# Kernel optimization log

Measured on AMD Instinct MI355X. Metric: run time of the kernel, lower is better.

## Reference

```python
import jax, jax.numpy as jnp
import numpy as np


def ternarize(w):
    """TWN ternarization: delta=0.7*mean|w|, alpha = mean of |w| over kept entries."""
    aw = jnp.abs(w)
    delta = 0.7 * jnp.mean(aw)
    mask = (aw > delta).astype(w.dtype)
    alpha = jnp.sum(aw * mask) / jnp.maximum(jnp.sum(mask), 1.0)
    return alpha * jnp.sign(w) * mask


def conv3x3(x, w):
    # NCHW input, OIHW weight, stride 1, padding 1
    return jax.lax.conv_general_dilated(
        x, w, window_strides=(1, 1), padding=((1, 1), (1, 1)),
        dimension_numbers=("NCHW", "OIHW", "NCHW"))


def maxpool2(x):
    return jax.lax.reduce_window(
        x, -jnp.inf, jax.lax.max,
        window_dimensions=(1, 1, 2, 2), window_strides=(1, 1, 2, 2),
        padding="VALID")


def setup_inputs() -> dict:
    key = jax.random.key(0)
    ks = jax.random.split(key, 9)
    B = 4096
    return {
        "x":   jax.random.normal(ks[0], (B, 3, 32, 32), dtype=jnp.float32),
        "w1":  jax.random.normal(ks[1], (16, 3, 3, 3), dtype=jnp.float32) * 0.1,
        "b1":  jax.random.normal(ks[2], (16,), dtype=jnp.float32) * 0.01,
        "w2":  jax.random.normal(ks[3], (32, 16, 3, 3), dtype=jnp.float32) * 0.1,
        "b2":  jax.random.normal(ks[4], (32,), dtype=jnp.float32) * 0.01,
        "wf1": jax.random.normal(ks[5], (128, 32 * 8 * 8), dtype=jnp.float32) * 0.05,
        "bf1": jax.random.normal(ks[6], (128,), dtype=jnp.float32) * 0.01,
        "wf2": jax.random.normal(ks[7], (10, 128), dtype=jnp.float32) * 0.05,
        "bf2": jax.random.normal(ks[8], (10,), dtype=jnp.float32) * 0.01,
    }


def reference(x, w1, b1, w2, b2, wf1, bf1, wf2, bf2):
    h = jax.nn.relu(conv3x3(x, ternarize(w1)) + b1[None, :, None, None])
    h = maxpool2(h)                                    # [B,16,16,16]
    h = jax.nn.relu(conv3x3(h, ternarize(w2)) + b2[None, :, None, None])
    h = maxpool2(h)                                    # [B,32,8,8]
    h = h.reshape(-1, 32 * 8 * 8)
    h = jax.nn.relu(h @ ternarize(wf1).T + bf1)        # [B,128]
    return h @ ternarize(wf2).T + bf2                  # [B,10]
```

## Files before the change

kernel.cpp:

```cpp
#include <hip/hip_runtime.h>
#include <math.h>


typedef _Float16 half2v __attribute__((ext_vector_type(2)));
typedef _Float16 half4  __attribute__((ext_vector_type(4)));
typedef _Float16 half8  __attribute__((ext_vector_type(8)));
typedef float    f32x4  __attribute__((ext_vector_type(4)));
typedef unsigned u32x2  __attribute__((ext_vector_type(2)));

#define WF1_N 262144
#define WF1_SLICES 64
#define WF1_SLICE 4096

__device__ __forceinline__ float block_reduce_256(float v, float* red, int t) {
    red[t] = v; __syncthreads();
    for (int o = 128; o > 0; o >>= 1) {
        if (t < o) red[t] += red[t + o];
        __syncthreads();
    }
    float r = red[0]; __syncthreads();
    return r;
}

__device__ __forceinline__ unsigned pk16(float a, float b) {
    half2v h;
    h[0] = (_Float16)a;
    h[1] = (_Float16)b;
    return __builtin_bit_cast(unsigned, h);
}

__global__ void tern_stageA(const float* __restrict__ w1,
                            const float* __restrict__ w2,
                            const float* __restrict__ wf1,
                            const float* __restrict__ wf2,
                            _Float16* __restrict__ tw1f,
                            _Float16* __restrict__ tw2f,
                            float* __restrict__ twf2,
                            float* __restrict__ part_sum) {
    __shared__ float red[256];
    const int t = threadIdx.x;
    const int bid = blockIdx.x;

    if (bid < WF1_SLICES) {
        const float4* src = reinterpret_cast<const float4*>(wf1 + (size_t)bid * WF1_SLICE);
        float s = 0.f;
#pragma unroll
        for (int j = 0; j < 4; ++j) {
            const float4 v = src[t + j * 256];
            s += fabsf(v.x) + fabsf(v.y) + fabsf(v.z) + fabsf(v.w);
        }
        const float tot = block_reduce_256(s, red, t);
        if (t == 0) part_sum[bid] = tot;
        return;
    }

    const float* w;
    int n;
    const int which = bid - WF1_SLICES;
    switch (which) {
        case 0: w = w1;  n = 432;  break;
        case 1: w = w2;  n = 4608; break;
        default: w = wf2; n = 1280; break;
    }
    float s = 0.f;
    for (int i = t; i < n; i += 256) s += fabsf(w[i]);
    const float delta = 0.7f * block_reduce_256(s, red, t) / (float)n;
    float sa = 0.f, cnt = 0.f;
    for (int i = t; i < n; i += 256) {
        float a = fabsf(w[i]);
        if (a > delta) { sa += a; cnt += 1.f; }
    }
    const float tot_sa = block_reduce_256(sa, red, t);
    const float tot_cnt = block_reduce_256(cnt, red, t);
    const float alpha = tot_sa / fmaxf(tot_cnt, 1.0f);

    switch (which) {
        case 0:
            for (int o = t; o < 768; o += 256) {
                int j = o & 3;
                int l = (o >> 2) & 63;
                int m = o >> 8;
                int rho = m * 4 + (l >> 4);
                int co = l & 15;
                float v = 0.f;
                if (rho < 9 && j < 3) {
                    float wv = w1[co * 27 + (rho / 3) * 9 + (rho % 3) * 3 + j];
                    v = (fabsf(wv) > delta) ? copysignf(alpha, wv) : 0.f;
                }
                tw1f[o] = (_Float16)v;
            }
            break;
        case 1:
            for (int o = t; o < 4608; o += 256) {
                int j  = o & 3;
                int ll = (o >> 2) & 63;
                int nt = (o >> 8) & 1;
                int s9 = o >> 9;
                int ci = (ll >> 4) * 4 + j;
                int co = (ll & 15) + nt * 16;
                float wv = w2[(co * 16 + ci) * 9 + s9];
                float v = (fabsf(wv) > delta) ? copysignf(alpha, wv) : 0.f;
                tw2f[o] = (_Float16)v;
            }
            break;
        default:
            for (int o = t; o < 1280; o += 256) {
                float wv = wf2[o];
                twf2[o] = (fabsf(wv) > delta) ? copysignf(alpha, wv) : 0.f;
            }
            break;
    }
}

__global__ void tern_stageB(const float* __restrict__ wf1,
                            const float* __restrict__ part_sum,
                            float* __restrict__ part_sa,
                            float* __restrict__ part_cnt) {
    __shared__ float red[256];
    const int t = threadIdx.x;
    const int bid = blockIdx.x;

    float v = (t < WF1_SLICES) ? part_sum[t] : 0.f;
    const float delta = 0.7f * block_reduce_256(v, red, t) / (float)WF1_N;

    const float4* src = reinterpret_cast<const float4*>(wf1 + (size_t)bid * WF1_SLICE);
    float sa = 0.f, cnt = 0.f;
#pragma unroll
    for (int j = 0; j < 4; ++j) {
        const float4 w4 = src[t + j * 256];
        float a;
        a = fabsf(w4.x); if (a > delta) { sa += a; cnt += 1.f; }
        a = fabsf(w4.y); if (a > delta) { sa += a; cnt += 1.f; }
        a = fabsf(w4.z); if (a > delta) { sa += a; cnt += 1.f; }
        a = fabsf(w4.w); if (a > delta) { sa += a; cnt += 1.f; }
    }
    const float tot_sa = block_reduce_256(sa, red, t);
    const float tot_cnt = block_reduce_256(cnt, red, t);
    if (t == 0) { part_sa[bid] = tot_sa; part_cnt[bid] = tot_cnt; }
}

__global__ void tern_stageC(const float* __restrict__ wf1,
                            const float* __restrict__ part_sum,
                            const float* __restrict__ part_sa,
                            const float* __restrict__ part_cnt,
                            _Float16* __restrict__ twf1) {
    __shared__ float red[256];
    const int t = threadIdx.x;

    float v = (t < WF1_SLICES) ? part_sum[t] : 0.f;
    const float delta = 0.7f * block_reduce_256(v, red, t) / (float)WF1_N;
    v = (t < WF1_SLICES) ? part_sa[t] : 0.f;
    const float tot_sa = block_reduce_256(v, red, t);
    v = (t < WF1_SLICES) ? part_cnt[t] : 0.f;
    const float tot_cnt = block_reduce_256(v, red, t);
    const float alpha = tot_sa / fmaxf(tot_cnt, 1.0f);

    const int tid = blockIdx.x * 256 + t;
    const float4 w4 = reinterpret_cast<const float4*>(wf1)[tid];
    half4 hv;
    hv[0] = (_Float16)((fabsf(w4.x) > delta) ? copysignf(alpha, w4.x) : 0.f);
    hv[1] = (_Float16)((fabsf(w4.y) > delta) ? copysignf(alpha, w4.y) : 0.f);
    hv[2] = (_Float16)((fabsf(w4.z) > delta) ? copysignf(alpha, w4.z) : 0.f);
    hv[3] = (_Float16)((fabsf(w4.w) > delta) ? copysignf(alpha, w4.w) : 0.f);
    reinterpret_cast<half4*>(twf1)[tid] = hv;
}

#define H1P 18
#define PSZ 3472
#define H1SZ (18*18*H1P)

__global__ __launch_bounds__(256, 5)
void conv12_kernel(const float* __restrict__ x,
                   const float* __restrict__ b1,
                   const float* __restrict__ b2,
                   const _Float16* __restrict__ tw1f,
                   const _Float16* __restrict__ tw2f,
                   _Float16* __restrict__ h2p) {
    __shared__ __align__(16) _Float16 PA[PSZ];
    __shared__ __align__(16) _Float16 PB[PSZ];
    __shared__ __align__(16) _Float16 h1s[H1SZ];
    __shared__ __align__(16) _Float16 h2s[2048];
    __shared__ float b1s[16], b2s[32];

    const int t = threadIdx.x;
    const int b = blockIdx.x;
    const int wid = t >> 6, l = t & 63;

    float4 xv4[3];
    {
        const float4* xb4 = reinterpret_cast<const float4*>(x + (size_t)b * 3072);
#pragma unroll
        for (int j = 0; j < 3; ++j) xv4[j] = xb4[t + j * 256];
    }
    half4 bfr1[3];
#pragma unroll
    for (int m = 0; m < 3; ++m)
        bfr1[m] = *reinterpret_cast<const half4*>(tw1f + (size_t)(m * 64 + l) * 4);
    if (t < 16) b1s[t] = b1[t];
    if (t < 32) b2s[t] = b2[t];

    {
        const float4 z = {0.f, 0.f, 0.f, 0.f};
        float4* pa4 = reinterpret_cast<float4*>(PA);
        float4* pb4 = reinterpret_cast<float4*>(PB);
        float4* h14 = reinterpret_cast<float4*>(h1s);
        for (int i = t; i < PSZ * 2 / 16; i += 256) { pa4[i] = z; pb4[i] = z; }
        for (int i = t; i < H1SZ * 2 / 16; i += 256) h14[i] = z;
    }
    __syncthreads();

    {
#pragma unroll
        for (int j = 0; j < 3; ++j) {
            const int f = t + j * 256;
            const int c = f >> 8, rem = f & 255;
            const int iy = rem >> 3, ix = (rem & 7) << 2;
            const int idx = ((c * 34) + iy + 1) * 34 + 1 + ix;
            const float4 v = xv4[j];
            const unsigned w0 = __builtin_bit_cast(unsigned, __builtin_amdgcn_cvt_pkrtz(v.x, v.y));
            const unsigned w1 = __builtin_bit_cast(unsigned, __builtin_amdgcn_cvt_pkrtz(v.z, v.w));
            const half2v h0 = __builtin_bit_cast(half2v, w0);
            const half2v h1 = __builtin_bit_cast(half2v, w1);
            *reinterpret_cast<unsigned*>(&PB[idx - 1]) = w0;
            *reinterpret_cast<unsigned*>(&PB[idx + 1]) = w1;
            PA[idx] = h0[0];
            *reinterpret_cast<unsigned*>(&PA[idx + 1]) = (w0 >> 16) | (w1 << 16);
            PA[idx + 3] = h1[1];
        }
    }
    __syncthreads();

    {
        const int r15 = l & 15, g = l >> 4;
        const int p = r15 & 1;
        int laneIdx[3];
#pragma unroll
        for (int m = 0; m < 3; ++m) {
            int rho = m * 4 + g;
            if (rho > 8) rho = 0;
            const int c = rho / 3, ky = rho % 3;
            laneIdx[m] = ((c * 34 + ky) * 34 + r15 - p) >> 1;
        }
        const unsigned* basep = p ? reinterpret_cast<const unsigned*>(PB)
                                  : reinterpret_cast<const unsigned*>(PA);
        const float bia = b1s[r15];

#pragma unroll 1
        for (int i = 0; i < 8; ++i) {
            const int P = wid * 8 + i;
            const int py = P >> 1, xh = P & 1;
            const int x0 = xh * 16;
            f32x4 accA = {0.f, 0.f, 0.f, 0.f};
            f32x4 accB = {0.f, 0.f, 0.f, 0.f};
#pragma unroll
            for (int h2 = 0; h2 < 2; ++h2) {
                const int y = 2 * py + h2;
                const int uoff = (y * 34 + x0) >> 1;
                f32x4 acc = {0.f, 0.f, 0.f, 0.f};
#pragma unroll
                for (int m = 0; m < 3; ++m) {
                    const unsigned* q = basep + laneIdx[m] + uoff;
                    u32x2 d;
                    d.x = q[0];
                    d.y = q[1];
                    const half4 a = __builtin_bit_cast(half4, d);
                    acc = __builtin_amdgcn_mfma_f32_16x16x16f16(a, bfr1[m], acc, 0, 0, 0);
                }
                if (h2 == 0) accA = acc; else accB = acc;
            }
            float e0 = fmaxf(fmaxf(accA[0], accA[1]), fmaxf(accB[0], accB[1]));
            float e1 = fmaxf(fmaxf(accA[2], accA[3]), fmaxf(accB[2], accB[3]));
            e0 = fmaxf(e0 + bia, 0.f);
            e1 = fmaxf(e1 + bia, 0.f);
            const int px0 = xh * 8 + g * 2;
            const int pix = (py + 1) * 18 + (px0 + 1);
            h1s[pix * H1P + r15]       = (_Float16)e0;
            h1s[(pix + 1) * H1P + r15] = (_Float16)e1;
        }
    }

    half4 bfr[9][2];
#pragma unroll
    for (int s = 0; s < 9; ++s)
#pragma unroll
        for (int nt = 0; nt < 2; ++nt)
            bfr[s][nt] = *reinterpret_cast<const half4*>(
                tw2f + (size_t)((s * 2 + nt) * 64 + l) * 4);
    __syncthreads();

    {
        const int xq = l & 15, g = l >> 4;
        const unsigned* h1u = reinterpret_cast<const unsigned*>(h1s);
        float sav[2][2];
#pragma unroll
        for (int yy = 0; yy < 4; ++yy) {
            const int y = wid * 4 + yy;
            const unsigned* qb = h1u + (y * 18 + xq) * 9 + g * 2;
            f32x4 acc0 = {0.f, 0.f, 0.f, 0.f};
            f32x4 acc1 = {0.f, 0.f, 0.f, 0.f};
#pragma unroll
            for (int s = 0; s < 9; ++s) {
                const int dy = s / 3, dx = s % 3;
                const int off = (dy * 18 + dx) * 9;
                u32x2 d;
                d.x = qb[off];
                d.y = qb[off + 1];
                const half4 a = __builtin_bit_cast(half4, d);
                acc0 = __builtin_amdgcn_mfma_f32_16x16x16f16(a, bfr[s][0], acc0, 0, 0, 0);
                acc1 = __builtin_amdgcn_mfma_f32_16x16x16f16(a, bfr[s][1], acc1, 0, 0, 0);
            }
            const float p00 = fmaxf(acc0[0], acc0[1]);
            const float p01 = fmaxf(acc0[2], acc0[3]);
            const float p10 = fmaxf(acc1[0], acc1[1]);
            const float p11 = fmaxf(acc1[2], acc1[3]);
            if ((yy & 1) == 0) {
                sav[0][0] = p00; sav[0][1] = p01;
                sav[1][0] = p10; sav[1][1] = p11;
            } else {
                const int py = (wid * 4 + yy) >> 1;
                const float v00 = fmaxf(fmaxf(sav[0][0], p00) + b2s[xq], 0.f);
                const float v01 = fmaxf(fmaxf(sav[0][1], p01) + b2s[xq], 0.f);
                const float v10 = fmaxf(fmaxf(sav[1][0], p10) + b2s[xq + 16], 0.f);
                const float v11 = fmaxf(fmaxf(sav[1][1], p11) + b2s[xq + 16], 0.f);
                unsigned* h2u = reinterpret_cast<unsigned*>(h2s);
                h2u[xq * 32 + py * 4 + g]        = pk16(v00, v01);
                h2u[(xq + 16) * 32 + py * 4 + g] = pk16(v10, v11);
            }
        }
    }
    __syncthreads();

    {
        const float4 v = reinterpret_cast<const float4*>(h2s)[t];
        reinterpret_cast<float4*>(h2p + (size_t)b * 2048)[t] = v;
    }
}

__global__ __launch_bounds__(1024, 4)
void fc_kernel(const _Float16* __restrict__ h2p,
               const _Float16* __restrict__ twf1,
               const float* __restrict__ bf1,
               const float* __restrict__ twf2,
               const float* __restrict__ bf2,
               float* __restrict__ out) {
    __shared__ float red[8][2048];

    const int t = threadIdx.x;
    const int wid = t >> 6, l = t & 63;
    const int lx = l & 15, g = l >> 4;
    const int m0 = blockIdx.x * 16;

    f32x4 acc[8];
#pragma unroll
    for (int nt = 0; nt < 8; ++nt) acc[nt] = (f32x4){0.f, 0.f, 0.f, 0.f};

    const int kb = wid * 128;
#pragma unroll
    for (int it = 0; it < 4; ++it) {
        const int k0 = kb + it * 32;
        const half8 a = *reinterpret_cast<const half8*>(
            h2p + (size_t)(m0 + lx) * 2048 + k0 + g * 8);
#pragma unroll
        for (int nt = 0; nt < 8; ++nt) {
            const half8 bb = *reinterpret_cast<const half8*>(
                twf1 + (size_t)(nt * 16 + lx) * 2048 + k0 + g * 8);
            acc[nt] = __builtin_amdgcn_mfma_f32_16x16x32_f16(a, bb, acc[nt], 0, 0, 0);
        }
    }

    for (int h = 8; h >= 1; h >>= 1) {
        if (wid >= h && wid < 2 * h) {
            float* dst = &red[wid - h][0];
#pragma unroll
            for (int nt = 0; nt < 8; ++nt)
                *reinterpret_cast<f32x4*>(dst + nt * 256 + l * 4) = acc[nt];
        }
        __syncthreads();
        if (wid < h) {
            const float* srcp = &red[wid][0];
#pragma unroll
            for (int nt = 0; nt < 8; ++nt) {
                const f32x4 v = *reinterpret_cast<const f32x4*>(srcp + nt * 256 + l * 4);
                acc[nt] += v;
            }
        }
        __syncthreads();
    }

    if (wid == 0) {
#pragma unroll
        for (int nt = 0; nt < 8; ++nt) {
            const int col = nt * 16 + lx;
            const float bias = bf1[col];
#pragma unroll
            for (int r = 0; r < 4; ++r)
                red[0][(g * 4 + r) * 128 + col] = fmaxf(acc[nt][r] + bias, 0.f);
        }
    }
    __syncthreads();

    if (t < 160) {
        const int m = t / 10, n = t % 10;
        float a = bf2[n];
#pragma unroll 8
        for (int k = 0; k < 128; ++k) a += red[0][m * 128 + k] * twf2[n * 128 + k];
        out[(size_t)(m0 + m) * 10 + n] = a;
    }
}

extern "C" void kernel_launch(void* const* d_in, const int* in_sizes, int n_in,
                              void* d_out, int out_size, void* d_ws, size_t ws_size,
                              hipStream_t stream) {
    const float* x   = (const float*)d_in[0];
    const float* w1  = (const float*)d_in[1];
    const float* b1  = (const float*)d_in[2];
    const float* w2  = (const float*)d_in[3];
    const float* b2  = (const float*)d_in[4];
    const float* wf1 = (const float*)d_in[5];
    const float* bf1 = (const float*)d_in[6];
    const float* wf2 = (const float*)d_in[7];
    const float* bf2 = (const float*)d_in[8];
    float* out = (float*)d_out;
    const int B = in_sizes[0] / (3 * 32 * 32);

    char* ws = (char*)d_ws;
    _Float16*  tw1f  = (_Float16*)(ws + 0);
    _Float16*  tw2f  = (_Float16*)(ws + 1536);
    _Float16*  twf1  = (_Float16*)(ws + 10752);
    float*     twf2  = (float*)(ws + 535040);
    _Float16*  h2p   = (_Float16*)(ws + 540160);
    float*     part_sum = (float*)(ws + 17317376);
    float*     part_sa  = part_sum + 64;
    float*     part_cnt = part_sa + 64;

    tern_stageA<<<WF1_SLICES + 3, 256, 0, stream>>>(w1, w2, wf1, wf2,
                                                    tw1f, tw2f, twf2, part_sum);
    tern_stageB<<<WF1_SLICES, 256, 0, stream>>>(wf1, part_sum, part_sa, part_cnt);
    tern_stageC<<<256, 256, 0, stream>>>(wf1, part_sum, part_sa, part_cnt, twf1);
    conv12_kernel<<<B, 256, 0, stream>>>(x, b1, b2, tw1f, tw2f, h2p);
    fc_kernel<<<B / 16, 1024, 0, stream>>>(h2p, twf1, bf1, twf2, bf2, out);
}
```

Baseline: 74.84 us.

## Fuse three ternarization kernels into one cooperative kernel with grid syncs

Merges the three weight-ternarization launches into a single cooperative kernel of 67 blocks that uses grid.sync between the partial-sum, threshold-sum and quantize phases. Wave-level shuffle reductions replace the block reductions when reading the 64 partials. This is meant to cut kernel launch gaps and the inter-kernel dependency overhead on the small preprocessing stages. The trade-offs are grid-sync cost and a final quantize phase that now runs on 67 blocks instead of 256.

```diff
diff --git a/kernel.cpp b/kernel.cpp
--- a/kernel.cpp
+++ b/kernel.cpp
@@ -1,5 +1,8 @@
 #include <hip/hip_runtime.h>
+#include <hip/hip_cooperative_groups.h>
 #include <math.h>
+
+namespace cg = cooperative_groups;
 
 
 typedef _Float16 half2v __attribute__((ext_vector_type(2)));
@@ -22,6 +25,12 @@
     return r;
 }
 
+__device__ __forceinline__ float wave_sum64(float v) {
+#pragma unroll
+    for (int o = 32; o > 0; o >>= 1) v += __shfl_xor(v, o);
+    return v;
+}
+
 __device__ __forceinline__ unsigned pk16(float a, float b) {
     half2v h;
     h[0] = (_Float16)a;
@@ -29,17 +38,22 @@
     return __builtin_bit_cast(unsigned, h);
 }
 
-__global__ void tern_stageA(const float* __restrict__ w1,
-                            const float* __restrict__ w2,
-                            const float* __restrict__ wf1,
-                            const float* __restrict__ wf2,
-                            _Float16* __restrict__ tw1f,
-                            _Float16* __restrict__ tw2f,
-                            float* __restrict__ twf2,
-                            float* __restrict__ part_sum) {
+__global__ void tern_fused(const float* __restrict__ w1,
+                           const float* __restrict__ w2,
+                           const float* __restrict__ wf1,
+                           const float* __restrict__ wf2,
+                           _Float16* __restrict__ tw1f,
+                           _Float16* __restrict__ tw2f,
+                           float* __restrict__ twf2,
+                           _Float16* __restrict__ twf1,
+                           float* __restrict__ part_sum,
+                           float* __restrict__ part_sa,
+                           float* __restrict__ part_cnt) {
     __shared__ float red[256];
     const int t = threadIdx.x;
     const int bid = blockIdx.x;
+    const int l = t & 63;
+    cg::grid_group grid = cg::this_grid();
 
     if (bid < WF1_SLICES) {
         const float4* src = reinterpret_cast<const float4*>(wf1 + (size_t)bid * WF1_SLICE);
@@ -51,118 +65,101 @@
         }
         const float tot = block_reduce_256(s, red, t);
         if (t == 0) part_sum[bid] = tot;
-        return;
-    }
-
-    const float* w;
-    int n;
-    const int which = bid - WF1_SLICES;
-    switch (which) {
-        case 0: w = w1;  n = 432;  break;
-        case 1: w = w2;  n = 4608; break;
-        default: w = wf2; n = 1280; break;
-    }
-    float s = 0.f;
-    for (int i = t; i < n; i += 256) s += fabsf(w[i]);
-    const float delta = 0.7f * block_reduce_256(s, red, t) / (float)n;
-    float sa = 0.f, cnt = 0.f;
-    for (int i = t; i < n; i += 256) {
-        float a = fabsf(w[i]);
-        if (a > delta) { sa += a; cnt += 1.f; }
-    }
-    const float tot_sa = block_reduce_256(sa, red, t);
-    const float tot_cnt = block_reduce_256(cnt, red, t);
-    const float alpha = tot_sa / fmaxf(tot_cnt, 1.0f);
-
-    switch (which) {
-        case 0:
-            for (int o = t; o < 768; o += 256) {
-                int j = o & 3;
-                int l = (o >> 2) & 63;
-                int m = o >> 8;
-                int rho = m * 4 + (l >> 4);
-                int co = l & 15;
-                float v = 0.f;
-                if (rho < 9 && j < 3) {
-                    float wv = w1[co * 27 + (rho / 3) * 9 + (rho % 3) * 3 + j];
-                    v = (fabsf(wv) > delta) ? copysignf(alpha, wv) : 0.f;
+    } else {
+        const float* w;
+        int n;
+        const int which = bid - WF1_SLICES;
+        switch (which) {
+            case 0: w = w1;  n = 432;  break;
+            case 1: w = w2;  n = 4608; break;
+            default: w = wf2; n = 1280; break;
+        }
+        float s = 0.f;
+        for (int i = t; i < n; i += 256) s += fabsf(w[i]);
+        const float delta = 0.7f * block_reduce_256(s, red, t) / (float)n;
+        float sa = 0.f, cnt = 0.f;
+        for (int i = t; i < n; i += 256) {
+            float a = fabsf(w[i]);
+            if (a > delta) { sa += a; cnt += 1.f; }
+        }
+        const float tot_sa = block_reduce_256(sa, red, t);
+        const float tot_cnt = block_reduce_256(cnt, red, t);
+        const float alpha = tot_sa / fmaxf(tot_cnt, 1.0f);
+
+        switch (which) {
+            case 0:
+                for (int o = t; o < 768; o += 256) {
+                    int j = o & 3;
+                    int ll = (o >> 2) & 63;
+                    int m = o >> 8;
+                    int rho = m * 4 + (ll >> 4);
+                    int co = ll & 15;
+                    float v = 0.f;
+                    if (rho < 9 && j < 3) {
+                        float wv = w1[co * 27 + (rho / 3) * 9 + (rho % 3) * 3 + j];
+                        v = (fabsf(wv) > delta) ? copysignf(alpha, wv) : 0.f;
+                    }
+                    tw1f[o] = (_Float16)v;
                 }
-                tw1f[o] = (_Float16)v;
-            }
-            break;
-        case 1:
-            for (int o = t; o < 4608; o += 256) {
-                int j  = o & 3;
-                int ll = (o >> 2) & 63;
-                int nt = (o >> 8) & 1;
-                int s9 = o >> 9;
-                int ci = (ll >> 4) * 4 + j;
-                int co = (ll & 15) + nt * 16;
-                float wv = w2[(co * 16 + ci) * 9 + s9];
-                float v = (fabsf(wv) > delta) ? copysignf(alpha, wv) : 0.f;
-                tw2f[o] = (_Float16)v;
-            }
-            break;
-        default:
-            for (int o = t; o < 1280; o += 256) {
-                float wv = wf2[o];
-                twf2[o] = (fabsf(wv) > delta) ? copysignf(alpha, wv) : 0.f;
-            }
-            break;
-    }
-}
-
-__global__ void tern_stageB(const float* __restrict__ wf1,
-                            const float* __restrict__ part_sum,
-                            float* __restrict__ part_sa,
-                            float* __restrict__ part_cnt) {
-    __shared__ float red[256];
-    const int t = threadIdx.x;
-    const int bid = blockIdx.x;
-
-    float v = (t < WF1_SLICES) ? part_sum[t] : 0.f;
-    const float delta = 0.7f * block_reduce_256(v, red, t) / (float)WF1_N;
-
-    const float4* src = reinterpret_cast<const float4*>(wf1 + (size_t)bid * WF1_SLICE);
-    float sa = 0.f, cnt = 0.f;
-#pragma unroll
-    for (int j = 0; j < 4; ++j) {
-        const float4 w4 = src[t + j * 256];
-        float a;
-        a = fabsf(w4.x); if (a > delta) { sa += a; cnt += 1.f; }
-        a = fabsf(w4.y); if (a > delta) { sa += a; cnt += 1.f; }
-        a = fabsf(w4.z); if (a > delta) { sa += a; cnt += 1.f; }
-        a = fabsf(w4.w); if (a > delta) { sa += a; cnt += 1.f; }
-    }
-    const float tot_sa = block_reduce_256(sa, red, t);
-    const float tot_cnt = block_reduce_256(cnt, red, t);
-    if (t == 0) { part_sa[bid] = tot_sa; part_cnt[bid] = tot_cnt; }
-}
-
-__global__ void tern_stageC(const float* __restrict__ wf1,
-                            const float* __restrict__ part_sum,
-                            const float* __restrict__ part_sa,
-                            const float* __restrict__ part_cnt,
-                            _Float16* __restrict__ twf1) {
-    __shared__ float red[256];
-    const int t = threadIdx.x;
-
-    float v = (t < WF1_SLICES) ? part_sum[t] : 0.f;
-    const float delta = 0.7f * block_reduce_256(v, red, t) / (float)WF1_N;
-    v = (t < WF1_SLICES) ? part_sa[t] : 0.f;
-    const float tot_sa = block_reduce_256(v, red, t);
-    v = (t < WF1_SLICES) ? part_cnt[t] : 0.f;
-    const float tot_cnt = block_reduce_256(v, red, t);
-    const float alpha = tot_sa / fmaxf(tot_cnt, 1.0f);
-
-    const int tid = blockIdx.x * 256 + t;
-    const float4 w4 = reinterpret_cast<const float4*>(wf1)[tid];
-    half4 hv;
-    hv[0] = (_Float16)((fabsf(w4.x) > delta) ? copysignf(alpha, w4.x) : 0.f);
-    hv[1] = (_Float16)((fabsf(w4.y) > delta) ? copysignf(alpha, w4.y) : 0.f);
-    hv[2] = (_Float16)((fabsf(w4.z) > delta) ? copysignf(alpha, w4.z) : 0.f);
-    hv[3] = (_Float16)((fabsf(w4.w) > delta) ? copysignf(alpha, w4.w) : 0.f);
-    reinterpret_cast<half4*>(twf1)[tid] = hv;
+                break;
+            case 1:
+                for (int o = t; o < 4608; o += 256) {
+                    int j  = o & 3;
+                    int ll = (o >> 2) & 63;
+                    int nt = (o >> 8) & 1;
+                    int s9 = o >> 9;
+                    int ci = (ll >> 4) * 4 + j;
+                    int co = (ll & 15) + nt * 16;
+                    float wv = w2[(co * 16 + ci) * 9 + s9];
+                    float v = (fabsf(wv) > delta) ? copysignf(alpha, wv) : 0.f;
+                    tw2f[o] = (_Float16)v;
+                }
+                break;
+            default:
+                for (int o = t; o < 1280; o += 256) {
+                    float wv = wf2[o];
+                    twf2[o] = (fabsf(wv) > delta) ? copysignf(alpha, wv) : 0.f;
+                }
+                break;
+        }
+    }
+    grid.sync();
+
+    if (bid < WF1_SLICES) {
+        const float delta = 0.7f * wave_sum64(part_sum[l]) / (float)WF1_N;
+        const float4* src = reinterpret_cast<const float4*>(wf1 + (size_t)bid * WF1_SLICE);
+        float sa = 0.f, cnt = 0.f;
+#pragma unroll
+        for (int j = 0; j < 4; ++j) {
+            const float4 w4 = src[t + j * 256];
+            float a;
+            a = fabsf(w4.x); if (a > delta) { sa += a; cnt += 1.f; }
+            a = fabsf(w4.y); if (a > delta) { sa += a; cnt += 1.f; }
+            a = fabsf(w4.z); if (a > delta) { sa += a; cnt += 1.f; }
+            a = fabsf(w4.w); if (a > delta) { sa += a; cnt += 1.f; }
+        }
+        const float tot_sa = block_reduce_256(sa, red, t);
+        const float tot_cnt = block_reduce_256(cnt, red, t);
+        if (t == 0) { part_sa[bid] = tot_sa; part_cnt[bid] = tot_cnt; }
+    }
+    grid.sync();
+
+    {
+        const float delta = 0.7f * wave_sum64(part_sum[l]) / (float)WF1_N;
+        const float tot_sa = wave_sum64(part_sa[l]);
+        const float tot_cnt = wave_sum64(part_cnt[l]);
+        const float alpha = tot_sa / fmaxf(tot_cnt, 1.0f);
+
+        for (int idx = bid * 256 + t; idx < WF1_N / 4; idx += 67 * 256) {
+            const float4 w4 = reinterpret_cast<const float4*>(wf1)[idx];
+            half4 hv;
+            hv[0] = (_Float16)((fabsf(w4.x) > delta) ? copysignf(alpha, w4.x) : 0.f);
+            hv[1] = (_Float16)((fabsf(w4.y) > delta) ? copysignf(alpha, w4.y) : 0.f);
+            hv[2] = (_Float16)((fabsf(w4.z) > delta) ? copysignf(alpha, w4.z) : 0.f);
+            hv[3] = (_Float16)((fabsf(w4.w) > delta) ? copysignf(alpha, w4.w) : 0.f);
+            reinterpret_cast<half4*>(twf1)[idx] = hv;
+        }
+    }
 }
 
 #define H1P 18
@@ -433,10 +430,11 @@
     float*     part_sa  = part_sum + 64;
     float*     part_cnt = part_sa + 64;
 
-    tern_stageA<<<WF1_SLICES + 3, 256, 0, stream>>>(w1, w2, wf1, wf2,
-                                                    tw1f, tw2f, twf2, part_sum);
-    tern_stageB<<<WF1_SLICES, 256, 0, stream>>>(wf1, part_sum, part_sa, part_cnt);
-    tern_stageC<<<256, 256, 0, stream>>>(wf1, part_sum, part_sa, part_cnt, twf1);
+    void* targs[] = {(void*)&w1, (void*)&w2, (void*)&wf1, (void*)&wf2,
+                     (void*)&tw1f, (void*)&tw2f, (void*)&twf2, (void*)&twf1,
+                     (void*)&part_sum, (void*)&part_sa, (void*)&part_cnt};
+    hipLaunchCooperativeKernel((void*)tern_fused, dim3(WF1_SLICES + 3), dim3(256),
+                               targs, 0, stream);
     conv12_kernel<<<B, 256, 0, stream>>>(x, b1, b2, tw1f, tw2f, h2p);
     fc_kernel<<<B / 16, 1024, 0, stream>>>(h2p, twf1, bf1, twf2, bf2, out);
 }
```

Measured after the change: 104.5 us. 1.4x slower.

## Split FC1 across output columns per wave instead of split-K with LDS reduction

Applied to the files above, without the earlier changes.

The FC1 kernel now gives each of 8 waves a 16-column slice of the 128 outputs over the full K=2048, instead of splitting K across 16 waves and combining partials through a 128KB LDS tree reduction. This removes the multi-stage reduction, its barriers and the large shared buffer, which should allow more blocks to be resident. In exchange each wave runs a long serial MFMA chain with two accumulators, and each wave reloads the same A rows, raising global/L2 traffic for activations.

```diff
diff --git a/kernel.cpp b/kernel.cpp
--- a/kernel.cpp
+++ b/kernel.cpp
@@ -336,66 +336,41 @@
     }
 }
 
-__global__ __launch_bounds__(1024, 4)
+__global__ __launch_bounds__(512, 2)
 void fc_kernel(const _Float16* __restrict__ h2p,
                const _Float16* __restrict__ twf1,
                const float* __restrict__ bf1,
                const float* __restrict__ twf2,
                const float* __restrict__ bf2,
                float* __restrict__ out) {
-    __shared__ float red[8][2048];
+    __shared__ float Hs[16][132];
 
     const int t = threadIdx.x;
     const int wid = t >> 6, l = t & 63;
     const int lx = l & 15, g = l >> 4;
     const int m0 = blockIdx.x * 16;
 
-    f32x4 acc[8];
-#pragma unroll
-    for (int nt = 0; nt < 8; ++nt) acc[nt] = (f32x4){0.f, 0.f, 0.f, 0.f};
-
-    const int kb = wid * 128;
-#pragma unroll
-    for (int it = 0; it < 4; ++it) {
-        const int k0 = kb + it * 32;
-        const half8 a = *reinterpret_cast<const half8*>(
-            h2p + (size_t)(m0 + lx) * 2048 + k0 + g * 8);
-#pragma unroll
-        for (int nt = 0; nt < 8; ++nt) {
-            const half8 bb = *reinterpret_cast<const half8*>(
-                twf1 + (size_t)(nt * 16 + lx) * 2048 + k0 + g * 8);
-            acc[nt] = __builtin_amdgcn_mfma_f32_16x16x32_f16(a, bb, acc[nt], 0, 0, 0);
-        }
-    }
-
-    for (int h = 8; h >= 1; h >>= 1) {
-        if (wid >= h && wid < 2 * h) {
-            float* dst = &red[wid - h][0];
-#pragma unroll
-            for (int nt = 0; nt < 8; ++nt)
-                *reinterpret_cast<f32x4*>(dst + nt * 256 + l * 4) = acc[nt];
-        }
-        __syncthreads();
-        if (wid < h) {
-            const float* srcp = &red[wid][0];
-#pragma unroll
-            for (int nt = 0; nt < 8; ++nt) {
-                const f32x4 v = *reinterpret_cast<const f32x4*>(srcp + nt * 256 + l * 4);
-                acc[nt] += v;
-            }
-        }
-        __syncthreads();
-    }
-
-    if (wid == 0) {
-#pragma unroll
-        for (int nt = 0; nt < 8; ++nt) {
-            const int col = nt * 16 + lx;
-            const float bias = bf1[col];
-#pragma unroll
-            for (int r = 0; r < 4; ++r)
-                red[0][(g * 4 + r) * 128 + col] = fmaxf(acc[nt][r] + bias, 0.f);
-        }
+    const _Float16* arow = h2p + (size_t)(m0 + lx) * 2048 + g * 8;
+    const _Float16* brow = twf1 + (size_t)(wid * 16 + lx) * 2048 + g * 8;
+
+    f32x4 acc0 = {0.f, 0.f, 0.f, 0.f};
+    f32x4 acc1 = {0.f, 0.f, 0.f, 0.f};
+#pragma unroll 8
+    for (int k0 = 0; k0 < 2048; k0 += 64) {
+        const half8 a0 = *reinterpret_cast<const half8*>(arow + k0);
+        const half8 b0 = *reinterpret_cast<const half8*>(brow + k0);
+        const half8 a1 = *reinterpret_cast<const half8*>(arow + k0 + 32);
+        const half8 b1 = *reinterpret_cast<const half8*>(brow + k0 + 32);
+        acc0 = __builtin_amdgcn_mfma_f32_16x16x32_f16(a0, b0, acc0, 0, 0, 0);
+        acc1 = __builtin_amdgcn_mfma_f32_16x16x32_f16(a1, b1, acc1, 0, 0, 0);
+    }
+
+    {
+        const int col = wid * 16 + lx;
+        const float bias = bf1[col];
+#pragma unroll
+        for (int r = 0; r < 4; ++r)
+            Hs[g * 4 + r][col] = fmaxf(acc0[r] + acc1[r] + bias, 0.f);
     }
     __syncthreads();
 
@@ -403,7 +378,7 @@
         const int m = t / 10, n = t % 10;
         float a = bf2[n];
 #pragma unroll 8
-        for (int k = 0; k < 128; ++k) a += red[0][m * 128 + k] * twf2[n * 128 + k];
+        for (int k = 0; k < 128; ++k) a += Hs[m][k] * twf2[n * 128 + k];
         out[(size_t)(m0 + m) * 10 + n] = a;
     }
 }
@@ -438,5 +413,5 @@
     tern_stageB<<<WF1_SLICES, 256, 0, stream>>>(wf1, part_sum, part_sa, part_cnt);
     tern_stageC<<<256, 256, 0, stream>>>(wf1, part_sum, part_sa, part_cnt, twf1);
     conv12_kernel<<<B, 256, 0, stream>>>(x, b1, b2, tw1f, tw2f, h2p);
-    fc_kernel<<<B / 16, 1024, 0, stream>>>(h2p, twf1, bf1, twf2, bf2, out);
-}
+    fc_kernel<<<B / 16, 512, 0, stream>>>(h2p, twf1, bf1, twf2, bf2, out);
+}
```

Measured after the change: 85.94 us. 1.15x slower.

## Store wf1 as unit sign ternary and apply alpha scale in FC epilogue

Applied to the files above, without the earlier changes.

Stage B now writes the fc1 weights directly as fp16 values in {-1,0,+1} while it computes the partial sums for alpha. The separate stage C kernel is removed, and the global alpha is reduced inside fc_kernel and applied to the accumulator before bias and ReLU. This drops one kernel launch and one extra pass over wf1, at the cost of a small per-block reduction in the FC kernel. Results change slightly in rounding because alpha is no longer folded into the fp16 weights.

```diff
diff --git a/kernel.cpp b/kernel.cpp
--- a/kernel.cpp
+++ b/kernel.cpp
@@ -20,6 +20,12 @@
     }
     float r = red[0]; __syncthreads();
     return r;
+}
+
+__device__ __forceinline__ float wave_sum64(float v) {
+#pragma unroll
+    for (int o = 32; o > 0; o >>= 1) v += __shfl_xor(v, o);
+    return v;
 }
 
 __device__ __forceinline__ unsigned pk16(float a, float b) {
@@ -115,7 +121,8 @@
 __global__ void tern_stageB(const float* __restrict__ wf1,
                             const float* __restrict__ part_sum,
                             float* __restrict__ part_sa,
-                            float* __restrict__ part_cnt) {
+                            float* __restrict__ part_cnt,
+                            _Float16* __restrict__ twf1) {
     __shared__ float red[256];
     const int t = threadIdx.x;
     const int bid = blockIdx.x;
@@ -124,45 +131,26 @@
     const float delta = 0.7f * block_reduce_256(v, red, t) / (float)WF1_N;
 
     const float4* src = reinterpret_cast<const float4*>(wf1 + (size_t)bid * WF1_SLICE);
+    half4* dst = reinterpret_cast<half4*>(twf1 + (size_t)bid * WF1_SLICE);
     float sa = 0.f, cnt = 0.f;
 #pragma unroll
     for (int j = 0; j < 4; ++j) {
         const float4 w4 = src[t + j * 256];
+        half4 hv;
         float a;
         a = fabsf(w4.x); if (a > delta) { sa += a; cnt += 1.f; }
+        hv[0] = (_Float16)((fabsf(w4.x) > delta) ? copysignf(1.0f, w4.x) : 0.f);
         a = fabsf(w4.y); if (a > delta) { sa += a; cnt += 1.f; }
+        hv[1] = (_Float16)((fabsf(w4.y) > delta) ? copysignf(1.0f, w4.y) : 0.f);
         a = fabsf(w4.z); if (a > delta) { sa += a; cnt += 1.f; }
+        hv[2] = (_Float16)((fabsf(w4.z) > delta) ? copysignf(1.0f, w4.z) : 0.f);
         a = fabsf(w4.w); if (a > delta) { sa += a; cnt += 1.f; }
+        hv[3] = (_Float16)((fabsf(w4.w) > delta) ? copysignf(1.0f, w4.w) : 0.f);
+        dst[t + j * 256] = hv;
     }
     const float tot_sa = block_reduce_256(sa, red, t);
     const float tot_cnt = block_reduce_256(cnt, red, t);
     if (t == 0) { part_sa[bid] = tot_sa; part_cnt[bid] = tot_cnt; }
-}
-
-__global__ void tern_stageC(const float* __restrict__ wf1,
-                            const float* __restrict__ part_sum,
-                            const float* __restrict__ part_sa,
-                            const float* __restrict__ part_cnt,
-                            _Float16* __restrict__ twf1) {
-    __shared__ float red[256];
-    const int t = threadIdx.x;
-
-    float v = (t < WF1_SLICES) ? part_sum[t] : 0.f;
-    const float delta = 0.7f * block_reduce_256(v, red, t) / (float)WF1_N;
-    v = (t < WF1_SLICES) ? part_sa[t] : 0.f;
-    const float tot_sa = block_reduce_256(v, red, t);
-    v = (t < WF1_SLICES) ? part_cnt[t] : 0.f;
-    const float tot_cnt = block_reduce_256(v, red, t);
-    const float alpha = tot_sa / fmaxf(tot_cnt, 1.0f);
-
-    const int tid = blockIdx.x * 256 + t;
-    const float4 w4 = reinterpret_cast<const float4*>(wf1)[tid];
-    half4 hv;
-    hv[0] = (_Float16)((fabsf(w4.x) > delta) ? copysignf(alpha, w4.x) : 0.f);
-    hv[1] = (_Float16)((fabsf(w4.y) > delta) ? copysignf(alpha, w4.y) : 0.f);
-    hv[2] = (_Float16)((fabsf(w4.z) > delta) ? copysignf(alpha, w4.z) : 0.f);
-    hv[3] = (_Float16)((fabsf(w4.w) > delta) ? copysignf(alpha, w4.w) : 0.f);
-    reinterpret_cast<half4*>(twf1)[tid] = hv;
 }
 
 #define H1P 18
@@ -339,6 +327,8 @@
 __global__ __launch_bounds__(1024, 4)
 void fc_kernel(const _Float16* __restrict__ h2p,
                const _Float16* __restrict__ twf1,
+               const float* __restrict__ part_sa,
+               const float* __restrict__ part_cnt,
                const float* __restrict__ bf1,
                const float* __restrict__ twf2,
                const float* __restrict__ bf2,
@@ -350,6 +340,13 @@
     const int lx = l & 15, g = l >> 4;
     const int m0 = blockIdx.x * 16;
 
+    float alphaW = 0.f;
+    if (wid == 0) {
+        const float tsa = wave_sum64(part_sa[l]);
+        const float tcn = wave_sum64(part_cnt[l]);
+        alphaW = tsa / fmaxf(tcn, 1.0f);
+    }
+
     f32x4 acc[8];
 #pragma unroll
     for (int nt = 0; nt < 8; ++nt) acc[nt] = (f32x4){0.f, 0.f, 0.f, 0.f};
@@ -394,7 +391,7 @@
             const float bias = bf1[col];
 #pragma unroll
             for (int r = 0; r < 4; ++r)
-                red[0][(g * 4 + r) * 128 + col] = fmaxf(acc[nt][r] + bias, 0.f);
+                red[0][(g * 4 + r) * 128 + col] = fmaxf(acc[nt][r] * alphaW + bias, 0.f);
         }
     }
     __syncthreads();
@@ -435,8 +432,8 @@
 
     tern_stageA<<<WF1_SLICES + 3, 256, 0, stream>>>(w1, w2, wf1, wf2,
                                                     tw1f, tw2f, twf2, part_sum);
-    tern_stageB<<<WF1_SLICES, 256, 0, stream>>>(wf1, part_sum, part_sa, part_cnt);
-    tern_stageC<<<256, 256, 0, stream>>>(wf1, part_sum, part_sa, part_cnt, twf1);
+    tern_stageB<<<WF1_SLICES, 256, 0, stream>>>(wf1, part_sum, part_sa, part_cnt, twf1);
     conv12_kernel<<<B, 256, 0, stream>>>(x, b1, b2, tw1f, tw2f, h2p);
-    fc_kernel<<<B / 16, 1024, 0, stream>>>(h2p, twf1, bf1, twf2, bf2, out);
-}
+    fc_kernel<<<B / 16, 1024, 0, stream>>>(h2p, twf1, part_sa, part_cnt,
+                                           bf1, twf2, bf2, out);
+}
```

New measurement: 71.23 us. -4.8%, faster.
